# Optimization experiments

Measured on AMD Instinct MI355X. Metric: run time of the kernel, lower is better.

## Reference

```python
import jax, jax.numpy as jnp
import numpy as np

C = 128; H = 56; W = 56; WS = 7; SS = 3; NH = 4; T = 8; B = 4
BT = B * T; L = H * W; N = WS * WS; HD = C // NH; SCALE = HD ** -0.5
NW = (H // WS) * (W // WS)

def _np_consts():
    # spatial relative position index (Swin)
    coords = np.stack(np.meshgrid(np.arange(WS), np.arange(WS), indexing='ij')).reshape(2, -1)
    rel = (coords[:, :, None] - coords[:, None, :]).transpose(1, 2, 0)
    rel[..., 0] += WS - 1; rel[..., 1] += WS - 1; rel[..., 0] *= 2 * WS - 1
    rpi = rel.sum(-1)  # (N, N) in [0, (2WS-1)^2)
    # temporal relative index
    tri = (np.arange(T)[:, None] - np.arange(T)[None, :]) + T - 1  # (T, T)
    # shifted-window attention mask
    img = np.zeros((1, H, W, 1), np.float32); cnt = 0
    sl = (slice(0, -WS), slice(-WS, -SS), slice(-SS, None))
    for hs in sl:
        for ws_ in sl:
            img[:, hs, ws_, :] = cnt; cnt += 1
    mw = img.reshape(1, H // WS, WS, W // WS, WS, 1).transpose(0, 1, 3, 2, 4, 5).reshape(-1, N)
    am = mw[:, None, :] - mw[:, :, None]
    attn_mask = np.where(am != 0, -100.0, 0.0).astype(np.float32)  # (NW, N, N)
    return rpi, tri, attn_mask

RPI, TRI, ATTN_MASK_NP = _np_consts()

def _ln(x, g, b, eps=1e-5):
    m = x.mean(-1, keepdims=True)
    v = ((x - m) ** 2).mean(-1, keepdims=True)
    return (x - m) * jax.lax.rsqrt(v + eps) * g + b

def _attn(x, bias, mask, qkv_w, qkv_b, proj_w, proj_b):
    # x: (Bn, n, C); bias: (NH, n, n); mask: (NW, n, n) or None
    Bn, n, _ = x.shape
    qkv = (x @ qkv_w + qkv_b).reshape(Bn, n, 3, NH, HD).transpose(2, 0, 3, 1, 4)
    q, k, v = qkv[0] * SCALE, qkv[1], qkv[2]  # (Bn, NH, n, HD)
    a = jnp.einsum('bhnd,bhmd->bhnm', q, k) + bias[None]
    if mask is not None:
        nW = mask.shape[0]
        a = (a.reshape(Bn // nW, nW, NH, n, n) + mask[None, :, None]).reshape(Bn, NH, n, n)
    a = jax.nn.softmax(a, axis=-1)
    o = jnp.einsum('bhnm,bhmd->bhnd', a, v).transpose(0, 2, 1, 3).reshape(Bn, n, C)
    return o @ proj_w + proj_b

def _fwd(x, qkv_w, qkv_b, proj_w, proj_b, rpb_table, tpb_table,
         norm1_g, norm1_b, norm2_g, norm2_b,
         mlp_w1, mlp_b1, mlp_w2, mlp_b2,
         s_w1, s_b1, s_w2, s_b2,
         t_w1, t_b1, t_w2, t_b2,
         a_w1, a_b1, a_w2, a_b2):
    gelu = lambda z: jax.nn.gelu(z, approximate=False)
    mask = jnp.asarray(ATTN_MASK_NP)
    sp_bias = rpb_table[RPI.reshape(-1)].reshape(N, N, NH).transpose(2, 0, 1)  # (NH,N,N)
    tp_bias = tpb_table[TRI.reshape(-1)].reshape(T, T, NH).transpose(2, 0, 1)  # (NH,T,T)

    # ---- temporal attention (t_attn=True, signal='video') ----
    shortcut = x
    xt = x.reshape(B, T, L, C).transpose(0, 2, 1, 3).reshape(B * L, T, C)
    xt = _ln(xt, norm1_g, norm1_b)
    xt = _attn(xt, tp_bias, None, qkv_w, qkv_b, proj_w, proj_b)
    # T_Adapter (non-residual)
    xt = gelu(xt @ t_w1 + t_b1) @ t_w2 + t_b2
    xt = xt.reshape(B, L, T, C).transpose(0, 2, 1, 3).reshape(BT, L, C)
    x = shortcut + xt

    # ---- shifted-window spatial attention ----
    shortcut = x
    xs = _ln(x, norm1_g, norm1_b).reshape(BT, H, W, C)
    xs = jnp.roll(xs, (-SS, -SS), axis=(1, 2))
    # window partition -> (BT*NW, N, C)
    xw = xs.reshape(BT, H // WS, WS, W // WS, WS, C).transpose(0, 1, 3, 2, 4, 5).reshape(-1, N, C)
    aw = _attn(xw, sp_bias, mask, qkv_w, qkv_b, proj_w, proj_b)
    # S_Adapter (SAdapter2, residual inside)
    aw = aw + (gelu(aw @ s_w1 + s_b1) @ s_w2 + s_b2)
    # window reverse
    xs = aw.reshape(BT, H // WS, W // WS, WS, WS, C).transpose(0, 1, 3, 2, 4, 5).reshape(BT, H, W, C)
    xs = jnp.roll(xs, (SS, SS), axis=(1, 2)).reshape(BT, L, C)
    x = shortcut + xs

    # ---- MLP + MLP_Adapter (AIM-style, scaled 0.5) ----
    xn = _ln(x, norm2_g, norm2_b)
    mlp = (gelu(xn @ mlp_w1 + mlp_b1)) @ mlp_w2 + mlp_b2
    ada = (gelu(xn @ a_w1 + a_b1)) @ a_w2 + a_b2
    return x + mlp + 0.5 * ada

def setup_inputs() -> dict:
    key = jax.random.key(0)
    ks = iter(jax.random.split(key, 16))
    p = lambda *s: jax.random.normal(next(ks), s, jnp.float32) * 0.02
    Ah = C // 4; M = 4 * C
    return {
        'x': jax.random.normal(next(ks), (BT, L, C), jnp.float32),
        'qkv_w': p(C, 3 * C), 'qkv_b': jnp.zeros((3 * C,), jnp.float32),
        'proj_w': p(C, C), 'proj_b': jnp.zeros((C,), jnp.float32),
        'rpb_table': p((2 * WS - 1) ** 2, NH), 'tpb_table': p(2 * T - 1, NH),
        'norm1_g': jnp.ones((C,), jnp.float32), 'norm1_b': jnp.zeros((C,), jnp.float32),
        'norm2_g': jnp.ones((C,), jnp.float32), 'norm2_b': jnp.zeros((C,), jnp.float32),
        'mlp_w1': p(C, M), 'mlp_b1': jnp.zeros((M,), jnp.float32),
        'mlp_w2': p(M, C), 'mlp_b2': jnp.zeros((C,), jnp.float32),
        's_w1': p(C, Ah), 's_b1': jnp.zeros((Ah,), jnp.float32),
        's_w2': p(Ah, C), 's_b2': jnp.zeros((C,), jnp.float32),
        't_w1': p(C, Ah), 't_b1': jnp.zeros((Ah,), jnp.float32),
        't_w2': p(Ah, C), 't_b2': jnp.zeros((C,), jnp.float32),
        'a_w1': p(C, Ah), 'a_b1': jnp.zeros((Ah,), jnp.float32),
        'a_w2': p(Ah, C), 'a_b2': jnp.zeros((C,), jnp.float32),
    }

def reference(x, qkv_w, qkv_b, proj_w, proj_b, rpb_table, tpb_table,
              norm1_g, norm1_b, norm2_g, norm2_b,
              mlp_w1, mlp_b1, mlp_w2, mlp_b2,
              s_w1, s_b1, s_w2, s_b2,
              t_w1, t_b1, t_w2, t_b2,
              a_w1, a_b1, a_w2, a_b2):
    return _fwd(x, qkv_w, qkv_b, proj_w, proj_b, rpb_table, tpb_table,
                norm1_g, norm1_b, norm2_g, norm2_b,
                mlp_w1, mlp_b1, mlp_w2, mlp_b2,
                s_w1, s_b1, s_w2, s_b2,
                t_w1, t_b1, t_w2, t_b2,
                a_w1, a_b1, a_w2, a_b2)
```

## Files before the change

kernel.cpp:

```cpp
#include <hip/hip_runtime.h>

#define TOKS 100352
#define LDIM 3136
#define SCALE_F 0.17677669529663687f

typedef unsigned short u16;
typedef u16   u16x8 __attribute__((ext_vector_type(8)));
typedef short s16x8 __attribute__((ext_vector_type(8)));
typedef float f32x8 __attribute__((ext_vector_type(8)));
typedef float f32x4 __attribute__((ext_vector_type(4)));

__device__ __forceinline__ float bf2f(u16 u){ return __uint_as_float(((unsigned)u)<<16); }
__device__ __forceinline__ u16 f2bf(float f){
  unsigned u = __float_as_uint(f);
  return (u16)((u + 0x7FFFu + ((u>>16)&1u)) >> 16);
}
__device__ __forceinline__ unsigned cvtpk(float a, float b){
  unsigned r;
  asm("v_cvt_pk_bf16_f32 %0, %1, %2" : "=v"(r) : "v"(a), "v"(b));
  return r;
}
__device__ __forceinline__ f32x8 ldbf8(const u16* p){
  u16x8 u = *(const u16x8*)p;
  f32x8 f;
  #pragma unroll
  for (int j=0;j<8;j++) f[j] = bf2f(u[j]);
  return f;
}
__device__ __forceinline__ u16x8 pack8(f32x8 v){
  u16x8 r;
  #pragma unroll
  for (int j=0;j<8;j++) r[j] = f2bf(v[j]);
  return r;
}
__device__ __forceinline__ float sum8(f32x8 a){
  return ((a[0]+a[1])+(a[2]+a[3]))+((a[4]+a[5])+(a[6]+a[7]));
}
__device__ __forceinline__ float gelu_f(float x){
  return x / (1.0f + __expf(-1.702f*x));
}

__device__ __forceinline__ void gl16(const u16* g, u16* l){
  __builtin_amdgcn_global_load_lds(
      (const __attribute__((address_space(1))) unsigned*)(const void*)g,
      (__attribute__((address_space(3))) unsigned*)(void*)l, 16, 0, 0);
}
__device__ __forceinline__ void stage_tile(const u16* __restrict__ src, size_t rowstart,
    int KTOT, int koff, u16* lds, int wv, int lane){
  const int rr = wv*4 + (lane>>4);
  const int sl = lane&15;
  const int kb = sl ^ (rr&7);
  const u16* g0 = src + (rowstart + rr)*(size_t)KTOT + koff + kb*8;
  u16* l0 = lds + wv*4*128;
  #pragma unroll
  for (int it=0; it<8; it++)
    gl16(g0 + (size_t)it*16*KTOT, l0 + it*16*128);
}

struct WSrc { const float* p[10]; };
__global__ __launch_bounds__(256) void prep_w(WSrc s, u16* __restrict__ dst){
  const int Ks[10]={128,128,128,512,128,32,128,32,128,32};
  const int Ns[10]={384,128,512,128,32,128,32,128,32,128};
  const int off[11]={0,49152,65536,131072,196608,200704,204800,208896,212992,217088,221184};
  int idx = blockIdx.x*256+threadIdx.x;
  int m=0;
  #pragma unroll
  for (int i=0;i<10;i++) if (idx>=off[i+1]) m=i+1;
  int e = idx-off[m];
  int K=Ks[m], Nn=Ns[m];
  int n=e/K, k=e-n*K;
  dst[idx] = f2bf(s.p[m][k*Nn+n]);
}

__global__ __launch_bounds__(256) void ln_kernel(const float* __restrict__ x,
    const float* __restrict__ g, const float* __restrict__ bta, u16* __restrict__ out)
{
  int tok  = (int)((blockIdx.x*256u + threadIdx.x) >> 6);
  int lane = threadIdx.x & 63;
  const float* xr = x + (size_t)tok*128;
  float v0 = xr[lane], v1 = xr[lane+64];
  float s = v0+v1;
  #pragma unroll
  for (int o=32;o;o>>=1) s += __shfl_xor(s,o);
  float m = s*(1.0f/128.0f);
  float d0=v0-m, d1=v1-m;
  float q = d0*d0+d1*d1;
  #pragma unroll
  for (int o=32;o;o>>=1) q += __shfl_xor(q,o);
  float rs = rsqrtf(q*(1.0f/128.0f)+1e-5f);
  u16* orow = out + (size_t)tok*128;
  orow[lane]    = f2bf(d0*rs*g[lane]   + bta[lane]);
  orow[lane+64] = f2bf(d1*rs*g[lane+64]+ bta[lane+64]);
}

template<int KCH, int NTC, int EPI>
__global__ __launch_bounds__(256,2) void gemm_tile(
    const u16* __restrict__ X, const u16* __restrict__ WT,
    const float* __restrict__ bias, void* outp, int N,
    const float* res1, const u16* __restrict__ adab)
{
  constexpr int KTOT = KCH*128;
  __shared__ u16 As[128*128];
  __shared__ u16 Bs[128*128];
  const int tid = threadIdx.x;
  const int wv = tid>>6, lane = tid&63, lr = lane>>4, lc = lane&15;
  const int wr = wv>>1, wc = wv&1;
  const size_t row0 = (size_t)blockIdx.x*128;

  f32x4 acc[4][4];
  #pragma unroll
  for (int mi=0;mi<4;mi++)
    #pragma unroll
    for (int nj=0;nj<4;nj++) acc[mi][nj] = (f32x4){0.f,0.f,0.f,0.f};

  for (int kc=0; kc<KCH; kc++){
    for (int nt=0; nt<NTC; nt++){
      if (kc+nt > 0) __syncthreads();
      if (nt == 0) stage_tile(X, row0, KTOT, kc*128, As, wv, lane);
      stage_tile(WT, (size_t)nt*128, KTOT, kc*128, Bs, wv, lane);
      __syncthreads();
      #pragma unroll
      for (int kt=0; kt<4; kt++){
        s16x8 af[4], bfr[4];
        #pragma unroll
        for (int mi=0;mi<4;mi++){
          int row = wr*64 + mi*16 + lc;
          af[mi] = *(const s16x8*)&As[row*128 + (((kt*4+lr) ^ (lc&7))*8)];
        }
        #pragma unroll
        for (int nj=0;nj<4;nj++){
          int col = wc*64 + nj*16 + lc;
          bfr[nj] = *(const s16x8*)&Bs[col*128 + (((kt*4+lr) ^ (lc&7))*8)];
        }
        #pragma unroll
        for (int mi=0;mi<4;mi++)
          #pragma unroll
          for (int nj=0;nj<4;nj++)
            acc[mi][nj] = __builtin_amdgcn_mfma_f32_16x16x32_bf16(bfr[nj], af[mi], acc[mi][nj], 0,0,0);
      }
      if (KCH==1){
        #pragma unroll
        for (int nj=0;nj<4;nj++){
          const int colb = nt*128 + wc*64 + nj*16 + lr*4;
          float4 b4 = *(const float4*)&bias[colb];
          #pragma unroll
          for (int mi=0;mi<4;mi++){
            const size_t row = row0 + wr*64 + mi*16 + lc;
            float v0=acc[mi][nj][0]+b4.x, v1=acc[mi][nj][1]+b4.y,
                  v2=acc[mi][nj][2]+b4.z, v3=acc[mi][nj][3]+b4.w;
            if constexpr (EPI==1){ v0=gelu_f(v0); v1=gelu_f(v1); v2=gelu_f(v2); v3=gelu_f(v3); }
            uint2 pk; pk.x = cvtpk(v0,v1); pk.y = cvtpk(v2,v3);
            *(uint2*)&((u16*)outp)[row*(size_t)N + colb] = pk;
            acc[mi][nj] = (f32x4){0.f,0.f,0.f,0.f};
          }
        }
      }
    }
  }
  if (KCH>1){
    #pragma unroll
    for (int nj=0;nj<4;nj++){
      const int colb = wc*64 + nj*16 + lr*4;
      float4 b4 = *(const float4*)&bias[colb];
      #pragma unroll
      for (int mi=0;mi<4;mi++){
        const size_t row = row0 + wr*64 + mi*16 + lc;
        float4 o4 = *(const float4*)&res1[row*128 + colb];
        uint2 au = *(const uint2*)&adab[row*128 + colb];
        float4 v;
        v.x = acc[mi][nj][0]+b4.x+o4.x+0.5f*bf2f((u16)(au.x&0xffff));
        v.y = acc[mi][nj][1]+b4.y+o4.y+0.5f*bf2f((u16)(au.x>>16));
        v.z = acc[mi][nj][2]+b4.z+o4.z+0.5f*bf2f((u16)(au.y&0xffff));
        v.w = acc[mi][nj][3]+b4.w+o4.w+0.5f*bf2f((u16)(au.y>>16));
        *(float4*)&((float*)outp)[row*128 + colb] = v;
      }
    }
  }
}

template<int SMODE>
__global__ __launch_bounds__(256,2) void proj_ada_tile(
    const u16* __restrict__ O, const u16* __restrict__ PW, const float* __restrict__ pb,
    const u16* __restrict__ W1T, const float* __restrict__ b1,
    const u16* __restrict__ W2T, const float* __restrict__ b2,
    const float* __restrict__ res1, float* __restrict__ outp,
    const float* __restrict__ gn, const float* __restrict__ gb, u16* __restrict__ xnout)
{
  __shared__ u16 As[128*128];
  __shared__ u16 Bs[128*128];
  __shared__ u16 Hs[4][32][40];
  const int tid = threadIdx.x;
  const int wv = tid>>6, lane = tid&63, lr = lane>>4, lc = lane&15;
  const int wr = wv>>1, wc = wv&1;
  const size_t row0 = (size_t)blockIdx.x*128;
  stage_tile(O, row0, 128, 0, As, wv, lane);
  stage_tile(PW, 0, 128, 0, Bs, wv, lane);
  __syncthreads();
  f32x4 acc[4][4];
  #pragma unroll
  for (int mi=0;mi<4;mi++)
    #pragma unroll
    for (int nj=0;nj<4;nj++) acc[mi][nj] = (f32x4){0.f,0.f,0.f,0.f};
  #pragma unroll
  for (int kt=0; kt<4; kt++){
    s16x8 af[4], bfr[4];
    #pragma unroll
    for (int mi=0;mi<4;mi++)
      af[mi] = *(const s16x8*)&As[(wr*64+mi*16+lc)*128 + (((kt*4+lr) ^ (lc&7))*8)];
    #pragma unroll
    for (int nj=0;nj<4;nj++)
      bfr[nj] = *(const s16x8*)&Bs[(wc*64+nj*16+lc)*128 + (((kt*4+lr) ^ (lc&7))*8)];
    #pragma unroll
    for (int mi=0;mi<4;mi++)
      #pragma unroll
      for (int nj=0;nj<4;nj++)
        acc[mi][nj] = __builtin_amdgcn_mfma_f32_16x16x32_bf16(bfr[nj], af[mi], acc[mi][nj], 0,0,0);
  }
  __syncthreads();
  #pragma unroll
  for (int nj=0;nj<4;nj++){
    const int colb = wc*64 + nj*16 + lr*4;
    float4 b4 = *(const float4*)&pb[colb];
    #pragma unroll
    for (int mi=0;mi<4;mi++){
      const int row = wr*64 + mi*16 + lc;
      uint2 pk;
      pk.x = cvtpk(acc[mi][nj][0]+b4.x, acc[mi][nj][1]+b4.y);
      pk.y = cvtpk(acc[mi][nj][2]+b4.z, acc[mi][nj][3]+b4.w);
      *(uint2*)&As[row*128 + (((colb>>3) ^ (row&7))*8) + (colb&7)] = pk;
    }
  }
  __syncthreads();
  const int rbase = wv*32;
  f32x4 a2[2][2];
  #pragma unroll
  for (int mi=0;mi<2;mi++){ a2[mi][0]=(f32x4){0.f,0.f,0.f,0.f}; a2[mi][1]=(f32x4){0.f,0.f,0.f,0.f}; }
  #pragma unroll
  for (int kt=0; kt<4; kt++){
    s16x8 af0 = *(const s16x8*)&As[(rbase+lc)*128 + (((kt*4+lr) ^ (lc&7))*8)];
    s16x8 af1 = *(const s16x8*)&As[(rbase+16+lc)*128 + (((kt*4+lr) ^ (lc&7))*8)];
    #pragma unroll
    for (int nj=0; nj<2; nj++){
      s16x8 b = *(const s16x8*)&W1T[(size_t)(nj*16+lc)*128 + kt*32 + lr*8];
      a2[0][nj] = __builtin_amdgcn_mfma_f32_16x16x32_bf16(b, af0, a2[0][nj], 0,0,0);
      a2[1][nj] = __builtin_amdgcn_mfma_f32_16x16x32_bf16(b, af1, a2[1][nj], 0,0,0);
    }
  }
  #pragma unroll
  for (int nj=0;nj<2;nj++){
    const int hb = nj*16 + lr*4;
    float4 b4 = *(const float4*)&b1[hb];
    #pragma unroll
    for (int mi=0;mi<2;mi++){
      const int tok = mi*16 + lc;
      uint2 pk;
      pk.x = cvtpk(gelu_f(a2[mi][nj][0]+b4.x), gelu_f(a2[mi][nj][1]+b4.y));
      pk.y = cvtpk(gelu_f(a2[mi][nj][2]+b4.z), gelu_f(a2[mi][nj][3]+b4.w));
      *(uint2*)&Hs[wv][tok][hb] = pk;
    }
  }
  f32x4 a3[2][8];
  #pragma unroll
  for (int mi=0;mi<2;mi++){
    s16x8 af = *(const s16x8*)&Hs[wv][mi*16+lc][lr*8];
    #pragma unroll
    for (int nj=0;nj<8;nj++){
      s16x8 b = *(const s16x8*)&W2T[(size_t)(nj*16+lc)*32 + lr*8];
      a3[mi][nj] = __builtin_amdgcn_mfma_f32_16x16x32_bf16(b, af, (f32x4){0.f,0.f,0.f,0.f}, 0,0,0);
    }
  }
  float sum[2]={0.f,0.f}, sq[2]={0.f,0.f};
  #pragma unroll
  for (int mi=0;mi<2;mi++){
    const int rl = rbase + mi*16 + lc;
    const size_t row = row0 + rl;
    #pragma unroll
    for (int nj=0;nj<8;nj++){
      const int colb = nj*16 + lr*4;
      float4 b4 = *(const float4*)&b2[colb];
      float4 r4 = *(const float4*)&res1[row*128 + colb];
      f32x4 v;
      v[0]=a3[mi][nj][0]+b4.x+r4.x; v[1]=a3[mi][nj][1]+b4.y+r4.y;
      v[2]=a3[mi][nj][2]+b4.z+r4.z; v[3]=a3[mi][nj][3]+b4.w+r4.w;
      if constexpr (SMODE==1){
        uint2 pu = *(const uint2*)&As[rl*128 + (((colb>>3) ^ (rl&7))*8) + (colb&7)];
        v[0] += bf2f((u16)(pu.x&0xffff)); v[1] += bf2f((u16)(pu.x>>16));
        v[2] += bf2f((u16)(pu.y&0xffff)); v[3] += bf2f((u16)(pu.y>>16));
      }
      float4 st; st.x=v[0]; st.y=v[1]; st.z=v[2]; st.w=v[3];
      *(float4*)&outp[row*128 + colb] = st;
      a3[mi][nj] = v;
      sum[mi] += (v[0]+v[1])+(v[2]+v[3]);
      sq[mi]  += (v[0]*v[0]+v[1]*v[1])+(v[2]*v[2]+v[3]*v[3]);
    }
  }
  #pragma unroll
  for (int mi=0;mi<2;mi++){
    float s2 = sum[mi], q2 = sq[mi];
    s2 += __shfl_xor(s2,16); s2 += __shfl_xor(s2,32);
    q2 += __shfl_xor(q2,16); q2 += __shfl_xor(q2,32);
    float mean = s2*(1.0f/128.0f);
    float var  = q2*(1.0f/128.0f) - mean*mean;
    float rs   = rsqrtf(var + 1e-5f);
    const size_t row = row0 + rbase + mi*16 + lc;
    #pragma unroll
    for (int nj=0;nj<8;nj++){
      const int colb = nj*16 + lr*4;
      float4 g4 = *(const float4*)&gn[colb];
      float4 h4 = *(const float4*)&gb[colb];
      uint2 pk;
      pk.x = cvtpk((a3[mi][nj][0]-mean)*rs*g4.x + h4.x,
                   (a3[mi][nj][1]-mean)*rs*g4.y + h4.y);
      pk.y = cvtpk((a3[mi][nj][2]-mean)*rs*g4.z + h4.z,
                   (a3[mi][nj][3]-mean)*rs*g4.w + h4.w);
      *(uint2*)&xnout[row*128 + colb] = pk;
    }
  }
}

__global__ __launch_bounds__(256,2) void mlp1_ada(
    const u16* __restrict__ X, const u16* __restrict__ WT, const float* __restrict__ bias,
    const u16* __restrict__ A1T, const float* __restrict__ ab1,
    const u16* __restrict__ A2T, const float* __restrict__ ab2,
    u16* __restrict__ Hout, u16* __restrict__ adab)
{
  __shared__ u16 As[128*128];
  __shared__ u16 Bs[128*128];
  __shared__ u16 Hs[4][32][40];
  const int tid = threadIdx.x;
  const int wv = tid>>6, lane = tid&63, lr = lane>>4, lc = lane&15;
  const int wr = wv>>1, wc = wv&1;
  const size_t row0 = (size_t)blockIdx.x*128;

  f32x4 acc[4][4];
  #pragma unroll
  for (int mi=0;mi<4;mi++)
    #pragma unroll
    for (int nj=0;nj<4;nj++) acc[mi][nj] = (f32x4){0.f,0.f,0.f,0.f};

  for (int nt=0; nt<4; nt++){
    if (nt > 0) __syncthreads();
    if (nt == 0) stage_tile(X, row0, 128, 0, As, wv, lane);
    stage_tile(WT, (size_t)nt*128, 128, 0, Bs, wv, lane);
    __syncthreads();
    #pragma unroll
    for (int kt=0; kt<4; kt++){
      s16x8 af[4], bfr[4];
      #pragma unroll
      for (int mi=0;mi<4;mi++)
        af[mi] = *(const s16x8*)&As[(wr*64+mi*16+lc)*128 + (((kt*4+lr) ^ (lc&7))*8)];
      #pragma unroll
      for (int nj=0;nj<4;nj++)
        bfr[nj] = *(const s16x8*)&Bs[(wc*64+nj*16+lc)*128 + (((kt*4+lr) ^ (lc&7))*8)];
      #pragma unroll
      for (int mi=0;mi<4;mi++)
        #pragma unroll
        for (int nj=0;nj<4;nj++)
          acc[mi][nj] = __builtin_amdgcn_mfma_f32_16x16x32_bf16(bfr[nj], af[mi], acc[mi][nj], 0,0,0);
    }
    #pragma unroll
    for (int nj=0;nj<4;nj++){
      const int colb = nt*128 + wc*64 + nj*16 + lr*4;
      float4 b4 = *(const float4*)&bias[colb];
      #pragma unroll
      for (int mi=0;mi<4;mi++){
        const size_t row = row0 + wr*64 + mi*16 + lc;
        uint2 pk;
        pk.x = cvtpk(gelu_f(acc[mi][nj][0]+b4.x), gelu_f(acc[mi][nj][1]+b4.y));
        pk.y = cvtpk(gelu_f(acc[mi][nj][2]+b4.z), gelu_f(acc[mi][nj][3]+b4.w));
        *(uint2*)&Hout[row*512 + colb] = pk;
        acc[mi][nj] = (f32x4){0.f,0.f,0.f,0.f};
      }
    }
  }
  const int rbase = wv*32;
  f32x4 a2[2][2];
  #pragma unroll
  for (int mi=0;mi<2;mi++){ a2[mi][0]=(f32x4){0.f,0.f,0.f,0.f}; a2[mi][1]=(f32x4){0.f,0.f,0.f,0.f}; }
  #pragma unroll
  for (int kt=0; kt<4; kt++){
    s16x8 af0 = *(const s16x8*)&As[(rbase+lc)*128 + (((kt*4+lr) ^ (lc&7))*8)];
    s16x8 af1 = *(const s16x8*)&As[(rbase+16+lc)*128 + (((kt*4+lr) ^ (lc&7))*8)];
    #pragma unroll
    for (int nj=0; nj<2; nj++){
      s16x8 b = *(const s16x8*)&A1T[(size_t)(nj*16+lc)*128 + kt*32 + lr*8];
      a2[0][nj] = __builtin_amdgcn_mfma_f32_16x16x32_bf16(b, af0, a2[0][nj], 0,0,0);
      a2[1][nj] = __builtin_amdgcn_mfma_f32_16x16x32_bf16(b, af1, a2[1][nj], 0,0,0);
    }
  }
  #pragma unroll
  for (int nj=0;nj<2;nj++){
    const int hb = nj*16 + lr*4;
    float4 b4 = *(const float4*)&ab1[hb];
    #pragma unroll
    for (int mi=0;mi<2;mi++){
      const int tok = mi*16 + lc;
      uint2 pk;
      pk.x = cvtpk(gelu_f(a2[mi][nj][0]+b4.x), gelu_f(a2[mi][nj][1]+b4.y));
      pk.y = cvtpk(gelu_f(a2[mi][nj][2]+b4.z), gelu_f(a2[mi][nj][3]+b4.w));
      *(uint2*)&Hs[wv][tok][hb] = pk;
    }
  }
  f32x4 a3[2][8];
  #pragma unroll
  for (int mi=0;mi<2;mi++){
    s16x8 af = *(const s16x8*)&Hs[wv][mi*16+lc][lr*8];
    #pragma unroll
    for (int nj=0;nj<8;nj++){
      s16x8 b = *(const s16x8*)&A2T[(size_t)(nj*16+lc)*32 + lr*8];
      a3[mi][nj] = __builtin_amdgcn_mfma_f32_16x16x32_bf16(b, af, (f32x4){0.f,0.f,0.f,0.f}, 0,0,0);
    }
  }
  #pragma unroll
  for (int nj=0;nj<8;nj++){
    const int colb = nj*16 + lr*4;
    float4 b4 = *(const float4*)&ab2[colb];
    #pragma unroll
    for (int mi=0;mi<2;mi++){
      const size_t row = row0 + rbase + mi*16 + lc;
      uint2 pk;
      pk.x = cvtpk(a3[mi][nj][0]+b4.x, a3[mi][nj][1]+b4.y);
      pk.y = cvtpk(a3[mi][nj][2]+b4.z, a3[mi][nj][3]+b4.w);
      *(uint2*)&adab[row*128 + colb] = pk;
    }
  }
}

__global__ __launch_bounds__(256) void t_attn_kernel(const u16* __restrict__ qkv,
    const float* __restrict__ tpb, u16* __restrict__ o)
{
  const int tid = threadIdx.x;
  const int li = tid>>5, h = (tid>>3)&3, t = tid&7;
  const int b = blockIdx.x/392, lt = blockIdx.x%392;
  const int l = lt*8+li;
  const size_t rowt = (size_t)(b*8+t)*LDIM + l;
  const u16* qp = qkv + rowt*384 + h*32;
  f32x8 q0 = ldbf8(qp)   *SCALE_F, q1 = ldbf8(qp+8) *SCALE_F,
        q2 = ldbf8(qp+16)*SCALE_F, q3 = ldbf8(qp+24)*SCALE_F;
  float s[8];
  #pragma unroll
  for (int t2=0;t2<8;t2++){
    const u16* kp = qkv + ((size_t)(b*8+t2)*LDIM + l)*384 + 128 + h*32;
    f32x8 d = q0*ldbf8(kp) + q1*ldbf8(kp+8) + q2*ldbf8(kp+16) + q3*ldbf8(kp+24);
    s[t2] = sum8(d) + tpb[(t-t2+7)*4 + h];
  }
  float m = s[0];
  #pragma unroll
  for (int t2=1;t2<8;t2++) m = fmaxf(m, s[t2]);
  float ssum = 0.f;
  #pragma unroll
  for (int t2=0;t2<8;t2++){ s[t2] = __expf(s[t2]-m); ssum += s[t2]; }
  const float inv = 1.0f/ssum;
  f32x8 o0={0,0,0,0,0,0,0,0}, o1={0,0,0,0,0,0,0,0},
        o2={0,0,0,0,0,0,0,0}, o3={0,0,0,0,0,0,0,0};
  #pragma unroll
  for (int t2=0;t2<8;t2++){
    const u16* vp = qkv + ((size_t)(b*8+t2)*LDIM + l)*384 + 256 + h*32;
    float aw = s[t2]*inv;
    o0 += aw*ldbf8(vp); o1 += aw*ldbf8(vp+8); o2 += aw*ldbf8(vp+16); o3 += aw*ldbf8(vp+24);
  }
  u16* op = o + rowt*128 + h*32;
  *(u16x8*)op      = pack8(o0); *(u16x8*)(op+8)  = pack8(o1);
  *(u16x8*)(op+16) = pack8(o2); *(u16x8*)(op+24) = pack8(o3);
}

__global__ __launch_bounds__(256,2) void s_attn_mfma(const u16* __restrict__ qkv,
    const float* __restrict__ rpb, u16* __restrict__ o)
{
  __shared__ u16 Qs[64][136];
  __shared__ u16 Ks[64][136];
  __shared__ u16 Vt[128][72];
  __shared__ float rpbL[676];
  __shared__ int rowL[49];
  __shared__ int codeL[49];
  const int tid = threadIdx.x;
  const int bidx = blockIdx.x;
  const int bt = bidx>>6, wh = (bidx>>3)&7, ww = bidx&7;
  if (tid < 49){
    int ph = tid/7, pwv = tid%7;
    int rh = wh*7+ph, rw = ww*7+pwv;
    int oh = rh+3; if (oh>=56) oh-=56;
    int ow = rw+3; if (ow>=56) ow-=56;
    rowL[tid] = bt*LDIM + oh*56 + ow;
    codeL[tid] = ((rh<49)?0:((rh<53)?1:2))*3 + ((rw<49)?0:((rw<53)?1:2));
  }
  for (int i2 = tid; i2 < 676; i2 += 256) rpbL[i2] = rpb[i2];
  for (int idx = tid; idx < 128*15; idx += 256){
    int d = idx/15, jj = 49 + (idx - d*15);
    Vt[d][jj] = 0;
  }
  __syncthreads();
  #pragma unroll
  for (int it = 0; it < 10; it++){
    int idx = it*256 + tid;
    if (idx < 2352){
      int j = idx/48, s = idx - j*48;
      const u16* src = qkv + (size_t)rowL[j]*384 + s*8;
      u16x8 v = *(const u16x8*)src;
      if (s < 16)      *(u16x8*)&Qs[j][s*8] = v;
      else if (s < 32) *(u16x8*)&Ks[j][(s-16)*8] = v;
      else { int c0 = (s-32)*8;
        #pragma unroll
        for (int e=0;e<8;e++) Vt[c0+e][j] = v[e];
      }
    }
  }
  __syncthreads();

  const int h = tid>>6, lane = tid&63, lr = lane>>4, lc = lane&15;
  s16x8 qf[4], kf[4];
  #pragma unroll
  for (int t=0;t<4;t++){
    qf[t] = *(const s16x8*)&Qs[t*16+lc][h*32+lr*8];
    kf[t] = *(const s16x8*)&Ks[t*16+lc][h*32+lr*8];
  }
  f32x4 sa[4][4];
  #pragma unroll
  for (int tj=0;tj<4;tj++){
    #pragma unroll
    for (int ti=0;ti<4;ti++)
      sa[tj][ti] = __builtin_amdgcn_mfma_f32_16x16x32_bf16(kf[tj], qf[ti], (f32x4){0.f,0.f,0.f,0.f}, 0,0,0);
  }
  int ihv[4], iwv[4], civ[4];
  #pragma unroll
  for (int ti=0;ti<4;ti++){
    int i = ti*16+lc; int im = (i<49)? i:48;
    int ih2 = (im*147)>>10; ihv[ti]=ih2; iwv[ti]=im-ih2*7; civ[ti]=codeL[im];
  }
  float rs[4] = {0.f,0.f,0.f,0.f};
  #pragma unroll
  for (int tj=0;tj<4;tj++){
    #pragma unroll
    for (int r=0;r<4;r++){
      int j = tj*16 + lr*4 + r;
      bool jv = (j<49);
      int jm = jv? j:48;
      int jh2 = (jm*147)>>10; int jw2 = jm - jh2*7; int cj = codeL[jm];
      #pragma unroll
      for (int ti=0;ti<4;ti++){
        float sv = sa[tj][ti][r]*SCALE_F
                 + rpbL[((ihv[ti]-jh2+6)*13 + (iwv[ti]-jw2+6))*4 + h];
        if (civ[ti] != cj) sv -= 100.f;
        float pv = jv ? __expf(sv) : 0.f;
        sa[tj][ti][r] = pv;
        rs[ti] += pv;
      }
    }
  }
  #pragma unroll
  for (int ti=0;ti<4;ti++){
    float t2 = rs[ti];
    t2 += __shfl_xor(t2, 16);
    t2 += __shfl_xor(t2, 32);
    rs[ti] = 1.0f/t2;
  }
  unsigned lo[4][4], hi[4][4];
  #pragma unroll
  for (int tj=0;tj<4;tj++){
    #pragma unroll
    for (int ti=0;ti<4;ti++){
      float inv = rs[ti];
      lo[tj][ti] = cvtpk(sa[tj][ti][0]*inv, sa[tj][ti][1]*inv);
      hi[tj][ti] = cvtpk(sa[tj][ti][2]*inv, sa[tj][ti][3]*inv);
    }
  }
  f32x4 oa[4][2];
  #pragma unroll
  for (int mi=0;mi<4;mi++){ oa[mi][0]=(f32x4){0.f,0.f,0.f,0.f}; oa[mi][1]=(f32x4){0.f,0.f,0.f,0.f}; }
  const int srcA = lc + ((lane>>4)&1)*32;
  const int srcB = srcA + 16;
  const bool hiHalf = (lr>=2);
  #pragma unroll
  for (int kt=0;kt<2;kt++){
    s16x8 vf[2];
    #pragma unroll
    for (int nd=0;nd<2;nd++)
      vf[nd] = *(const s16x8*)&Vt[h*32 + nd*16 + lc][kt*32 + lr*8];
    #pragma unroll
    for (int mi=0;mi<4;mi++){
      unsigned wA0 = __shfl(lo[2*kt][mi],   srcA), wB0 = __shfl(lo[2*kt+1][mi], srcA);
      unsigned wA1 = __shfl(hi[2*kt][mi],   srcA), wB1 = __shfl(hi[2*kt+1][mi], srcA);
      unsigned wA2 = __shfl(lo[2*kt][mi],   srcB), wB2 = __shfl(lo[2*kt+1][mi], srcB);
      unsigned wA3 = __shfl(hi[2*kt][mi],   srcB), wB3 = __shfl(hi[2*kt+1][mi], srcB);
      union { unsigned u[4]; s16x8 v8; } cv;
      cv.u[0] = hiHalf? wB0 : wA0;
      cv.u[1] = hiHalf? wB1 : wA1;
      cv.u[2] = hiHalf? wB2 : wA2;
      cv.u[3] = hiHalf? wB3 : wA3;
      #pragma unroll
      for (int nd=0;nd<2;nd++)
        oa[mi][nd] = __builtin_amdgcn_mfma_f32_16x16x32_bf16(cv.v8, vf[nd], oa[mi][nd], 0,0,0);
    }
  }
  #pragma unroll
  for (int mi=0;mi<4;mi++){
    #pragma unroll
    for (int r=0;r<4;r++){
      int i = mi*16 + lr*4 + r;
      if (i < 49){
        size_t orow = (size_t)rowL[i]*128 + h*32;
        o[orow + lc]      = f2bf(oa[mi][0][r]);
        o[orow + 16 + lc] = f2bf(oa[mi][1][r]);
      }
    }
  }
}

extern "C" void kernel_launch(void* const* d_in, const int* in_sizes, int n_in,
                              void* d_out, int out_size, void* d_ws, size_t ws_size,
                              hipStream_t stream)
{
  (void)in_sizes; (void)n_in; (void)out_size; (void)ws_size;
  const float* x      = (const float*)d_in[0];
  const float* qkv_w  = (const float*)d_in[1];
  const float* qkv_b  = (const float*)d_in[2];
  const float* proj_w = (const float*)d_in[3];
  const float* proj_b = (const float*)d_in[4];
  const float* rpb    = (const float*)d_in[5];
  const float* tpb    = (const float*)d_in[6];
  const float* n1g    = (const float*)d_in[7];
  const float* n1b    = (const float*)d_in[8];
  const float* n2g    = (const float*)d_in[9];
  const float* n2b    = (const float*)d_in[10];
  const float* mw1    = (const float*)d_in[11];
  const float* mb1    = (const float*)d_in[12];
  const float* mw2    = (const float*)d_in[13];
  const float* mb2    = (const float*)d_in[14];
  const float* sw1    = (const float*)d_in[15];
  const float* sb1    = (const float*)d_in[16];
  const float* sw2    = (const float*)d_in[17];
  const float* sb2    = (const float*)d_in[18];
  const float* tw1    = (const float*)d_in[19];
  const float* tb1    = (const float*)d_in[20];
  const float* tw2    = (const float*)d_in[21];
  const float* tb2    = (const float*)d_in[22];
  const float* aw1    = (const float*)d_in[23];
  const float* ab1    = (const float*)d_in[24];
  const float* aw2    = (const float*)d_in[25];
  const float* ab2    = (const float*)d_in[26];

  char* ws = (char*)d_ws;
  u16*   Xn  = (u16*)(ws);
  u16*   QKV = (u16*)(ws + 25690112ULL);
  u16*   O   = (u16*)(ws + 102760448ULL);
  float* Cb  = (float*)(ws + 134873088ULL);
  u16*   AdaBf = (u16*)(ws + 134873088ULL);
  u16*   WT  = (u16*)(ws + 186253312ULL);
  float* out = (float*)d_out;

  const u16 *WTqkv=WT, *WTproj=WT+49152, *WTm1=WT+65536, *WTm2=WT+131072,
            *WTt1=WT+196608, *WTt2=WT+200704, *WTs1=WT+204800, *WTs2=WT+208896,
            *WTa1=WT+212992, *WTa2=WT+217088;

  WSrc srcs; srcs.p[0]=qkv_w; srcs.p[1]=proj_w; srcs.p[2]=mw1; srcs.p[3]=mw2;
  srcs.p[4]=tw1; srcs.p[5]=tw2; srcs.p[6]=sw1; srcs.p[7]=sw2; srcs.p[8]=aw1; srcs.p[9]=aw2;
  prep_w<<<864,256,0,stream>>>(srcs, WT);

  ln_kernel<<<25088,256,0,stream>>>(x, n1g, n1b, Xn);
  gemm_tile<1,3,0><<<784,256,0,stream>>>(Xn, WTqkv, qkv_b, QKV, 384, nullptr,nullptr);
  t_attn_kernel<<<1568,256,0,stream>>>(QKV, tpb, O);
  proj_ada_tile<0><<<784,256,0,stream>>>(O, WTproj, proj_b, WTt1, tb1, WTt2, tb2,
                                          x, Cb, n1g, n1b, Xn);
  gemm_tile<1,3,0><<<784,256,0,stream>>>(Xn, WTqkv, qkv_b, QKV, 384, nullptr,nullptr);
  s_attn_mfma<<<2048,256,0,stream>>>(QKV, rpb, O);
  proj_ada_tile<1><<<784,256,0,stream>>>(O, WTproj, proj_b, WTs1, sb1, WTs2, sb2,
                                          Cb, out, n2g, n2b, Xn);
  mlp1_ada<<<784,256,0,stream>>>(Xn, WTm1, mb1, WTa1, ab1, WTa2, ab2, QKV, AdaBf);
  gemm_tile<4,1,4><<<784,256,0,stream>>>(QKV, WTm2, mb2, out, 128, out, AdaBf);
}
```

Before: 407.2 us.

## Fuse MLP fc1, fc2 and adapter into one kernel keeping hidden in LDS

Result: faster. 378.6 us (median of 2 runs) (-7.0%).

```diff
diff --git a/kernel.cpp b/kernel.cpp
--- a/kernel.cpp
+++ b/kernel.cpp
@@ -138,7 +138,7 @@
           for (int nj=0;nj<4;nj++)
             acc[mi][nj] = __builtin_amdgcn_mfma_f32_16x16x32_bf16(bfr[nj], af[mi], acc[mi][nj], 0,0,0);
       }
-      if (KCH==1){
+      {
         #pragma unroll
         for (int nj=0;nj<4;nj++){
           const int colb = nt*128 + wc*64 + nj*16 + lr*4;
@@ -157,25 +157,7 @@
       }
     }
   }
-  if (KCH>1){
-    #pragma unroll
-    for (int nj=0;nj<4;nj++){
-      const int colb = wc*64 + nj*16 + lr*4;
-      float4 b4 = *(const float4*)&bias[colb];
-      #pragma unroll
-      for (int mi=0;mi<4;mi++){
-        const size_t row = row0 + wr*64 + mi*16 + lc;
-        float4 o4 = *(const float4*)&res1[row*128 + colb];
-        uint2 au = *(const uint2*)&adab[row*128 + colb];
-        float4 v;
-        v.x = acc[mi][nj][0]+b4.x+o4.x+0.5f*bf2f((u16)(au.x&0xffff));
-        v.y = acc[mi][nj][1]+b4.y+o4.y+0.5f*bf2f((u16)(au.x>>16));
-        v.z = acc[mi][nj][2]+b4.z+o4.z+0.5f*bf2f((u16)(au.y&0xffff));
-        v.w = acc[mi][nj][3]+b4.w+o4.w+0.5f*bf2f((u16)(au.y>>16));
-        *(float4*)&((float*)outp)[row*128 + colb] = v;
-      }
-    }
-  }
+  (void)res1; (void)adab;
 }
 
 template<int SMODE>
@@ -318,31 +300,36 @@
   }
 }
 
-__global__ __launch_bounds__(256,2) void mlp1_ada(
-    const u16* __restrict__ X, const u16* __restrict__ WT, const float* __restrict__ bias,
+__global__ __launch_bounds__(256,2) void mlp_fused(
+    const u16* __restrict__ X, const u16* __restrict__ W1T, const float* __restrict__ b1,
+    const u16* __restrict__ W2T, const float* __restrict__ b2,
     const u16* __restrict__ A1T, const float* __restrict__ ab1,
     const u16* __restrict__ A2T, const float* __restrict__ ab2,
-    u16* __restrict__ Hout, u16* __restrict__ adab)
+    float* __restrict__ outp)
 {
   __shared__ u16 As[128*128];
   __shared__ u16 Bs[128*128];
-  __shared__ u16 Hs[4][32][40];
   const int tid = threadIdx.x;
   const int wv = tid>>6, lane = tid&63, lr = lane>>4, lc = lane&15;
   const int wr = wv>>1, wc = wv&1;
   const size_t row0 = (size_t)blockIdx.x*128;
 
-  f32x4 acc[4][4];
+  stage_tile(X, row0, 128, 0, As, wv, lane);
+  stage_tile(W1T, 0, 128, 0, Bs, wv, lane);
+  __syncthreads();
+
+  f32x4 oacc[4][4];
   #pragma unroll
   for (int mi=0;mi<4;mi++)
     #pragma unroll
-    for (int nj=0;nj<4;nj++) acc[mi][nj] = (f32x4){0.f,0.f,0.f,0.f};
-
-  for (int nt=0; nt<4; nt++){
-    if (nt > 0) __syncthreads();
-    if (nt == 0) stage_tile(X, row0, 128, 0, As, wv, lane);
-    stage_tile(WT, (size_t)nt*128, 128, 0, Bs, wv, lane);
-    __syncthreads();
+    for (int nj=0;nj<4;nj++) oacc[mi][nj] = (f32x4){0.f,0.f,0.f,0.f};
+
+  for (int ck=0; ck<4; ck++){
+    f32x4 acc[4][4];
+    #pragma unroll
+    for (int mi=0;mi<4;mi++)
+      #pragma unroll
+      for (int nj=0;nj<4;nj++) acc[mi][nj] = (f32x4){0.f,0.f,0.f,0.f};
     #pragma unroll
     for (int kt=0; kt<4; kt++){
       s16x8 af[4], bfr[4];
@@ -358,70 +345,103 @@
         for (int nj=0;nj<4;nj++)
           acc[mi][nj] = __builtin_amdgcn_mfma_f32_16x16x32_bf16(bfr[nj], af[mi], acc[mi][nj], 0,0,0);
     }
+    __syncthreads();
     #pragma unroll
     for (int nj=0;nj<4;nj++){
-      const int colb = nt*128 + wc*64 + nj*16 + lr*4;
-      float4 b4 = *(const float4*)&bias[colb];
+      const int hidb = wc*64 + nj*16 + lr*4;
+      float4 b4 = *(const float4*)&b1[ck*128 + hidb];
       #pragma unroll
       for (int mi=0;mi<4;mi++){
-        const size_t row = row0 + wr*64 + mi*16 + lc;
+        const int tok = wr*64 + mi*16 + lc;
         uint2 pk;
         pk.x = cvtpk(gelu_f(acc[mi][nj][0]+b4.x), gelu_f(acc[mi][nj][1]+b4.y));
         pk.y = cvtpk(gelu_f(acc[mi][nj][2]+b4.z), gelu_f(acc[mi][nj][3]+b4.w));
-        *(uint2*)&Hout[row*512 + colb] = pk;
-        acc[mi][nj] = (f32x4){0.f,0.f,0.f,0.f};
-      }
-    }
-  }
-  const int rbase = wv*32;
-  f32x4 a2[2][2];
-  #pragma unroll
-  for (int mi=0;mi<2;mi++){ a2[mi][0]=(f32x4){0.f,0.f,0.f,0.f}; a2[mi][1]=(f32x4){0.f,0.f,0.f,0.f}; }
+        *(uint2*)&Bs[tok*128 + (((hidb>>3) ^ (tok&7))*8) + (hidb&7)] = pk;
+      }
+    }
+    __syncthreads();
+    #pragma unroll
+    for (int kt=0; kt<4; kt++){
+      s16x8 hf[4], wf[4];
+      #pragma unroll
+      for (int mi=0;mi<4;mi++)
+        hf[mi] = *(const s16x8*)&Bs[(wr*64+mi*16+lc)*128 + (((kt*4+lr) ^ (lc&7))*8)];
+      #pragma unroll
+      for (int nj=0;nj<4;nj++)
+        wf[nj] = *(const s16x8*)&W2T[(size_t)(wc*64+nj*16+lc)*512 + ck*128 + kt*32 + lr*8];
+      #pragma unroll
+      for (int mi=0;mi<4;mi++)
+        #pragma unroll
+        for (int nj=0;nj<4;nj++)
+          oacc[mi][nj] = __builtin_amdgcn_mfma_f32_16x16x32_bf16(hf[mi], wf[nj], oacc[mi][nj], 0,0,0);
+    }
+    if (ck<3){
+      __syncthreads();
+      stage_tile(W1T, (size_t)(ck+1)*128, 128, 0, Bs, wv, lane);
+      __syncthreads();
+    }
+  }
+
+  f32x4 a2[4][2];
+  #pragma unroll
+  for (int mi=0;mi<4;mi++){ a2[mi][0]=(f32x4){0.f,0.f,0.f,0.f}; a2[mi][1]=(f32x4){0.f,0.f,0.f,0.f}; }
   #pragma unroll
   for (int kt=0; kt<4; kt++){
-    s16x8 af0 = *(const s16x8*)&As[(rbase+lc)*128 + (((kt*4+lr) ^ (lc&7))*8)];
-    s16x8 af1 = *(const s16x8*)&As[(rbase+16+lc)*128 + (((kt*4+lr) ^ (lc&7))*8)];
-    #pragma unroll
-    for (int nj=0; nj<2; nj++){
-      s16x8 b = *(const s16x8*)&A1T[(size_t)(nj*16+lc)*128 + kt*32 + lr*8];
-      a2[0][nj] = __builtin_amdgcn_mfma_f32_16x16x32_bf16(b, af0, a2[0][nj], 0,0,0);
-      a2[1][nj] = __builtin_amdgcn_mfma_f32_16x16x32_bf16(b, af1, a2[1][nj], 0,0,0);
-    }
-  }
-  #pragma unroll
-  for (int nj=0;nj<2;nj++){
-    const int hb = nj*16 + lr*4;
-    float4 b4 = *(const float4*)&ab1[hb];
-    #pragma unroll
-    for (int mi=0;mi<2;mi++){
-      const int tok = mi*16 + lc;
-      uint2 pk;
-      pk.x = cvtpk(gelu_f(a2[mi][nj][0]+b4.x), gelu_f(a2[mi][nj][1]+b4.y));
-      pk.y = cvtpk(gelu_f(a2[mi][nj][2]+b4.z), gelu_f(a2[mi][nj][3]+b4.w));
-      *(uint2*)&Hs[wv][tok][hb] = pk;
-    }
-  }
-  f32x4 a3[2][8];
-  #pragma unroll
-  for (int mi=0;mi<2;mi++){
-    s16x8 af = *(const s16x8*)&Hs[wv][mi*16+lc][lr*8];
-    #pragma unroll
-    for (int nj=0;nj<8;nj++){
-      s16x8 b = *(const s16x8*)&A2T[(size_t)(nj*16+lc)*32 + lr*8];
-      a3[mi][nj] = __builtin_amdgcn_mfma_f32_16x16x32_bf16(b, af, (f32x4){0.f,0.f,0.f,0.f}, 0,0,0);
-    }
-  }
-  #pragma unroll
-  for (int nj=0;nj<8;nj++){
-    const int colb = nj*16 + lr*4;
-    float4 b4 = *(const float4*)&ab2[colb];
-    #pragma unroll
-    for (int mi=0;mi<2;mi++){
-      const size_t row = row0 + rbase + mi*16 + lc;
-      uint2 pk;
-      pk.x = cvtpk(a3[mi][nj][0]+b4.x, a3[mi][nj][1]+b4.y);
-      pk.y = cvtpk(a3[mi][nj][2]+b4.z, a3[mi][nj][3]+b4.w);
-      *(uint2*)&adab[row*128 + colb] = pk;
+    s16x8 af[4];
+    #pragma unroll
+    for (int mi=0;mi<4;mi++)
+      af[mi] = *(const s16x8*)&As[(wr*64+mi*16+lc)*128 + (((kt*4+lr) ^ (lc&7))*8)];
+    s16x8 bA = *(const s16x8*)&A1T[(size_t)lc*128 + kt*32 + lr*8];
+    s16x8 bB = *(const s16x8*)&A1T[(size_t)(16+lc)*128 + kt*32 + lr*8];
+    #pragma unroll
+    for (int mi=0;mi<4;mi++){
+      a2[mi][0] = __builtin_amdgcn_mfma_f32_16x16x32_bf16(bA, af[mi], a2[mi][0], 0,0,0);
+      a2[mi][1] = __builtin_amdgcn_mfma_f32_16x16x32_bf16(bB, af[mi], a2[mi][1], 0,0,0);
+    }
+  }
+  __syncthreads();
+  if (wc==0){
+    #pragma unroll
+    for (int nj=0;nj<2;nj++){
+      const int hb = nj*16 + lr*4;
+      float4 b4 = *(const float4*)&ab1[hb];
+      #pragma unroll
+      for (int mi=0;mi<4;mi++){
+        const int tok = wr*64 + mi*16 + lc;
+        uint2 pk;
+        pk.x = cvtpk(0.5f*gelu_f(a2[mi][nj][0]+b4.x), 0.5f*gelu_f(a2[mi][nj][1]+b4.y));
+        pk.y = cvtpk(0.5f*gelu_f(a2[mi][nj][2]+b4.z), 0.5f*gelu_f(a2[mi][nj][3]+b4.w));
+        *(uint2*)&As[tok*64 + (((hb>>3) ^ (tok&7))*8) + (hb&7)] = pk;
+      }
+    }
+  }
+  __syncthreads();
+  {
+    s16x8 hqf[4];
+    #pragma unroll
+    for (int mi=0;mi<4;mi++){
+      const int tok = wr*64 + mi*16 + lc;
+      hqf[mi] = *(const s16x8*)&As[tok*64 + ((lr ^ (tok&7))*8)];
+    }
+    #pragma unroll
+    for (int nj=0;nj<4;nj++){
+      s16x8 a2f = *(const s16x8*)&A2T[(size_t)(wc*64+nj*16+lc)*32 + lr*8];
+      #pragma unroll
+      for (int mi=0;mi<4;mi++)
+        oacc[mi][nj] = __builtin_amdgcn_mfma_f32_16x16x32_bf16(hqf[mi], a2f, oacc[mi][nj], 0,0,0);
+    }
+  }
+  #pragma unroll
+  for (int nj=0;nj<4;nj++){
+    const int col = wc*64 + nj*16 + lc;
+    const float badd = b2[col] + 0.5f*ab2[col];
+    #pragma unroll
+    for (int mi=0;mi<4;mi++){
+      #pragma unroll
+      for (int r=0;r<4;r++){
+        const size_t row = row0 + wr*64 + mi*16 + lr*4 + r;
+        outp[row*128 + col] += oacc[mi][nj][r] + badd;
+      }
     }
   }
 }
@@ -644,7 +664,6 @@
   u16*   QKV = (u16*)(ws + 25690112ULL);
   u16*   O   = (u16*)(ws + 102760448ULL);
   float* Cb  = (float*)(ws + 134873088ULL);
-  u16*   AdaBf = (u16*)(ws + 134873088ULL);
   u16*   WT  = (u16*)(ws + 186253312ULL);
   float* out = (float*)d_out;
 
@@ -665,6 +684,5 @@
   s_attn_mfma<<<2048,256,0,stream>>>(QKV, rpb, O);
   proj_ada_tile<1><<<784,256,0,stream>>>(O, WTproj, proj_b, WTs1, sb1, WTs2, sb2,
                                           Cb, out, n2g, n2b, Xn);
-  mlp1_ada<<<784,256,0,stream>>>(Xn, WTm1, mb1, WTa1, ab1, WTa2, ab2, QKV, AdaBf);
-  gemm_tile<4,1,4><<<784,256,0,stream>>>(QKV, WTm2, mb2, out, 128, out, AdaBf);
-}
+  mlp_fused<<<784,256,0,stream>>>(Xn, WTm1, mb1, WTm2, mb2, WTa1, ab1, WTa2, ab2, out);
+}
```
